# Optimization experiments

Measured on AMD Instinct MI355X. Metric: run time of the kernel, lower is better.

The kernel has to match this reference:

```python
import jax, jax.numpy as jnp
import numpy as np

B, N, C, H = 4, 2048, 1024, 16
DH = C // H
SCALE = DH ** -0.5


def setup_inputs() -> dict:
    key = jax.random.key(0)
    ks = jax.random.split(key, 5)
    s = C ** -0.5
    return {
        "x": jax.random.normal(ks[0], (B, N, C), dtype=jnp.float32),
        "Wq": jax.random.normal(ks[1], (C, C), dtype=jnp.float32) * s,
        "Wkv": jax.random.normal(ks[2], (C, 2 * C), dtype=jnp.float32) * s,
        "Wout": jax.random.normal(ks[3], (C, C), dtype=jnp.float32) * s,
        "bout": jax.random.normal(ks[4], (C,), dtype=jnp.float32) * 0.01,
    }


def reference(x, Wq, Wkv, Wout, bout):
    b, n, c = x.shape
    # projections (torch Linear: x @ W.T, here we store W already as [in,out])
    q = (x @ Wq).reshape(b, n, H, DH).transpose(0, 2, 1, 3)  # b h n d
    kv = x @ Wkv
    k, v = jnp.split(kv, 2, axis=-1)
    k = k.reshape(b, n, H, DH).transpose(0, 2, 1, 3)
    v = v.reshape(b, n, H, DH).transpose(0, 2, 1, 3)
    sim = jnp.einsum("bhnd,bhmd->bhnm", q, k) * SCALE
    attn = jax.nn.softmax(sim, axis=-1)
    out = jnp.einsum("bhnm,bhmd->bhnd", attn, v)
    out = out.transpose(0, 2, 1, 3).reshape(b, n, c)
    return out @ Wout + bout
```

## Files before the change

### kernel.cpp

```cpp
#include <hip/hip_runtime.h>
#include <stdint.h>

typedef unsigned short u16;
typedef unsigned int u32;
typedef __attribute__((ext_vector_type(8))) short bf16x8;
typedef __attribute__((ext_vector_type(8))) unsigned short u16x8;
typedef __attribute__((ext_vector_type(4))) float f32x4;

#define B_DIM 4
#define N_DIM 2048
#define C_DIM 1024
#define H_DIM 16
#define M_DIM (B_DIM * N_DIM)
#define QSCALE 0.18033688011112042f

__device__ __forceinline__ u16 f2bf(float f) {
  u32 u = __builtin_bit_cast(u32, f);
  return (u16)((u + 0x7FFFu + ((u >> 16) & 1u)) >> 16);
}

__device__ __forceinline__ void gload16(const void* g, void* l) {
  __builtin_amdgcn_global_load_lds(
      (const __attribute__((address_space(1))) u32*)g,
      (__attribute__((address_space(3))) u32*)l, 16, 0, 0);
}

__global__ void cast_bf16_kernel(const float* __restrict__ in, u16* __restrict__ out, int n4) {
  int i = blockIdx.x * blockDim.x + threadIdx.x;
  int stride = gridDim.x * blockDim.x;
  for (; i < n4; i += stride) {
    float4 v = ((const float4*)in)[i];
    ushort4 o;
    o.x = f2bf(v.x); o.y = f2bf(v.y); o.z = f2bf(v.z); o.w = f2bf(v.w);
    ((ushort4*)out)[i] = o;
  }
}

__global__ void tcast_kernel(const float* __restrict__ W, u16* __restrict__ Wt, int K, int N) {
  __shared__ float tile[32][33];
  int n0 = blockIdx.x * 32, k0 = blockIdx.y * 32;
  int tx = threadIdx.x, ty = threadIdx.y;
  #pragma unroll
  for (int i = 0; i < 32; i += 8)
    tile[ty + i][tx] = W[(size_t)(k0 + ty + i) * N + (n0 + tx)];
  __syncthreads();
  #pragma unroll
  for (int i = 0; i < 32; i += 8)
    Wt[(size_t)(n0 + ty + i) * K + (k0 + tx)] = f2bf(tile[tx][ty + i]);
}

template <int MODE>
__global__ __launch_bounds__(256) void gemm_bt_kernel(
    const u16* __restrict__ A, const u16* __restrict__ Bt, void* __restrict__ Cout,
    const float* __restrict__ bias, u16* __restrict__ vt, u16* __restrict__ aux,
    int K, int N) {
  __shared__ __align__(16) char lds[16384];
  const int tid  = threadIdx.x;
  const int lane = tid & 63, w = tid >> 6;
  const int lr = lane & 15, g = lane >> 4;
  const int m0 = blockIdx.y * 128, n0 = blockIdx.x * 128;
  const int wm = w >> 1, wn = w & 1;

  f32x4 acc[4][4] = {};
  const int nkt = K >> 5;
  const int rsub = lane >> 2;
  const int csub = lane & 3;
  for (int kt = 0; kt < nkt; ++kt) {
    #pragma unroll
    for (int j = 0; j < 2; ++j) {
      int rowblk = w * 2 + j;
      int row = rowblk * 16 + rsub;
      gload16(A  + (size_t)(m0 + row) * K + kt * 32 + csub * 8, lds + rowblk * 1024);
      gload16(Bt + (size_t)(n0 + row) * K + kt * 32 + csub * 8, lds + 8192 + rowblk * 1024);
    }
    __syncthreads();
    bf16x8 a[4], b[4];
    #pragma unroll
    for (int m = 0; m < 4; ++m)
      a[m] = *(const bf16x8*)(lds + ((wm * 64 + m * 16 + lr) * 64 + g * 16));
    #pragma unroll
    for (int n = 0; n < 4; ++n)
      b[n] = *(const bf16x8*)(lds + 8192 + ((wn * 64 + n * 16 + lr) * 64 + g * 16));
    #pragma unroll
    for (int m = 0; m < 4; ++m)
      #pragma unroll
      for (int n = 0; n < 4; ++n)
        acc[m][n] = __builtin_amdgcn_mfma_f32_16x16x32_bf16(a[m], b[n], acc[m][n], 0, 0, 0);
    __syncthreads();
  }
  #pragma unroll
  for (int m = 0; m < 4; ++m) {
    #pragma unroll
    for (int n = 0; n < 4; ++n) {
      int col  = n0 + wn * 64 + n * 16 + lr;
      int row0 = m0 + wm * 64 + m * 16 + g * 4;
      if constexpr (MODE == 1) {
        #pragma unroll
        for (int r = 0; r < 4; ++r)
          ((float*)Cout)[(size_t)(row0 + r) * N + col] = acc[m][n][r] + bias[col];
      } else {
        if (col < 1024) {
          #pragma unroll
          for (int r = 0; r < 4; ++r)
            ((u16*)Cout)[(size_t)(row0 + r) * 1024 + col] = f2bf(acc[m][n][r] * QSCALE);
        } else if (col < 2048) {
          int cc = col - 1024;
          #pragma unroll
          for (int r = 0; r < 4; ++r)
            aux[(size_t)(row0 + r) * 1024 + cc] = f2bf(acc[m][n][r]);
        } else {
          int cc = col - 2048;
          int hh = cc >> 6, d = cc & 63;
          int bb = row0 >> 11, nn = row0 & 2047;
          ushort4 pkv;
          pkv.x = f2bf(acc[m][n][0]); pkv.y = f2bf(acc[m][n][1]);
          pkv.z = f2bf(acc[m][n][2]); pkv.w = f2bf(acc[m][n][3]);
          *(ushort4*)(vt + ((size_t)(bb * 16 + hh) * 64 + d) * 2048 + nn) = pkv;
        }
      }
    }
  }
}

__global__ __launch_bounds__(256) void attn_kernel(
    const u16* __restrict__ Qb, const u16* __restrict__ Kb,
    const u16* __restrict__ Vt, u16* __restrict__ AO) {
  __shared__ __align__(16) char lds[51200];
  const int tid  = threadIdx.x;
  const int lane = tid & 63, w = tid >> 6;
  const int lr = lane & 15, g = lane >> 4;
  const int lin = blockIdx.x;
  const int nid = (lin & 7) * 128 + (lin >> 3);
  const int bh = nid >> 4;
  const int b = bh >> 4, h = bh & 15;
  const int q0 = (nid & 15) * 128 + w * 32;
  const size_t rowbase = (size_t)b * N_DIM;

  bf16x8 qf[2][2];
  #pragma unroll
  for (int qs = 0; qs < 2; ++qs)
    #pragma unroll
    for (int kb = 0; kb < 2; ++kb)
      qf[qs][kb] = *(const bf16x8*)(Qb + (rowbase + q0 + qs * 16 + lr) * C_DIM + h * 64 + kb * 32 + g * 8);

  bf16x8 onesb;
  #pragma unroll
  for (int j = 0; j < 8; ++j) onesb[j] = (short)0x3F80;

  f32x4 accO[2][4] = {};
  f32x4 accSum[2] = {};
  char* Pl = lds + 32768 + w * 4608;

  auto STAGE = [&](int kt, int buf) {
    #pragma unroll
    for (int j = 0; j < 2; ++j) {
      int c = (w * 2 + j) * 64 + lane;
      int row = c >> 3, slot = (c & 7) ^ (row & 7);
      gload16(Kb + (size_t)(rowbase + kt * 64 + row) * 1024 + h * 64 + slot * 8,
              lds + buf * 8192 + (w * 2 + j) * 1024);
      gload16(Vt + ((size_t)bh * 64 + row) * 2048 + kt * 64 + slot * 8,
              lds + 16384 + buf * 8192 + (w * 2 + j) * 1024);
    }
  };

  STAGE(0, 0);
  __syncthreads();

  for (int kt = 0; kt < N_DIM / 64; ++kt) {
    if (kt + 1 < N_DIM / 64) STAGE(kt + 1, (kt + 1) & 1);
    const char* K_ = lds + (kt & 1) * 8192;
    const char* V_ = lds + 16384 + (kt & 1) * 8192;

    bf16x8 kfr[4][2];
    #pragma unroll
    for (int kf = 0; kf < 4; ++kf)
      #pragma unroll
      for (int kb = 0; kb < 2; ++kb)
        kfr[kf][kb] = *(const bf16x8*)(K_ + (kf * 16 + lr) * 128 + (((kb * 4 + g) ^ (lr & 7)) << 4));
    f32x4 st[2][4] = {};
    #pragma unroll
    for (int qs = 0; qs < 2; ++qs)
      #pragma unroll
      for (int kf = 0; kf < 4; ++kf)
        #pragma unroll
        for (int kb = 0; kb < 2; ++kb)
          st[qs][kf] = __builtin_amdgcn_mfma_f32_16x16x32_bf16(kfr[kf][kb], qf[qs][kb], st[qs][kf], 0, 0, 0);

    #pragma unroll
    for (int qs = 0; qs < 2; ++qs) {
      #pragma unroll
      for (int kf = 0; kf < 4; ++kf) {
        float e0 = __builtin_amdgcn_exp2f(st[qs][kf][0]);
        float e1 = __builtin_amdgcn_exp2f(st[qs][kf][1]);
        float e2 = __builtin_amdgcn_exp2f(st[qs][kf][2]);
        float e3 = __builtin_amdgcn_exp2f(st[qs][kf][3]);
        u32 r0, r1;
        asm("v_cvt_pk_bf16_f32 %0, %1, %2" : "=v"(r0) : "v"(e0), "v"(e1));
        asm("v_cvt_pk_bf16_f32 %0, %1, %2" : "=v"(r1) : "v"(e2), "v"(e3));
        uint2 pk; pk.x = r0; pk.y = r1;
        *(uint2*)(Pl + (qs * 16 + lr) * 144 + kf * 32 + g * 8) = pk;
      }
    }

    bf16x8 vfr[4][2];
    #pragma unroll
    for (int nf = 0; nf < 4; ++nf)
      #pragma unroll
      for (int kb = 0; kb < 2; ++kb)
        vfr[nf][kb] = *(const bf16x8*)(V_ + (nf * 16 + lr) * 128 + (((kb * 4 + g) ^ (lr & 7)) << 4));
    #pragma unroll
    for (int qs = 0; qs < 2; ++qs) {
      #pragma unroll
      for (int kb = 0; kb < 2; ++kb) {
        bf16x8 pa = *(const bf16x8*)(Pl + (qs * 16 + lr) * 144 + kb * 64 + g * 16);
        accSum[qs] = __builtin_amdgcn_mfma_f32_16x16x32_bf16(pa, onesb, accSum[qs], 0, 0, 0);
        #pragma unroll
        for (int nf = 0; nf < 4; ++nf)
          accO[qs][nf] = __builtin_amdgcn_mfma_f32_16x16x32_bf16(pa, vfr[nf][kb], accO[qs][nf], 0, 0, 0);
      }
    }
    __syncthreads();
  }

  #pragma unroll
  for (int qs = 0; qs < 2; ++qs)
    #pragma unroll
    for (int r = 0; r < 4; ++r) {
      float inv = __builtin_amdgcn_rcpf(accSum[qs][r]);
      int q = q0 + qs * 16 + 4 * g + r;
      #pragma unroll
      for (int nf = 0; nf < 4; ++nf)
        AO[(rowbase + q) * C_DIM + h * 64 + nf * 16 + lr] = f2bf(accO[qs][nf][r] * inv);
    }
}

extern "C" void kernel_launch(void* const* d_in, const int* in_sizes, int n_in,
                              void* d_out, int out_size, void* d_ws, size_t ws_size,
                              hipStream_t stream) {
  (void)in_sizes; (void)n_in; (void)out_size; (void)ws_size;
  const float* x    = (const float*)d_in[0];
  const float* Wq   = (const float*)d_in[1];
  const float* Wkv  = (const float*)d_in[2];
  const float* Wout = (const float*)d_in[3];
  const float* bout = (const float*)d_in[4];
  float* out = (float*)d_out;

  char* ws = (char*)d_ws;
  u16* xb   = (u16*)(ws);
  u16* wqT  = (u16*)(ws + (16u << 20));
  u16* wkvT = (u16*)(ws + (18u << 20));
  u16* woT  = (u16*)(ws + (22u << 20));
  u16* q    = (u16*)(ws + (24u << 20));
  u16* kbuf = (u16*)(ws + (40u << 20));
  u16* vT   = (u16*)(ws + (56u << 20));
  u16* ao   = xb;

  cast_bf16_kernel<<<2048, 256, 0, stream>>>(x, xb, M_DIM * C_DIM / 4);
  dim3 tb(32, 8);
  tcast_kernel<<<dim3(C_DIM / 32,     C_DIM / 32), tb, 0, stream>>>(Wq,   wqT,  C_DIM, C_DIM);
  tcast_kernel<<<dim3(2 * C_DIM / 32, C_DIM / 32), tb, 0, stream>>>(Wkv,  wkvT, C_DIM, 2 * C_DIM);
  tcast_kernel<<<dim3(C_DIM / 32,     C_DIM / 32), tb, 0, stream>>>(Wout, woT,  C_DIM, C_DIM);

  gemm_bt_kernel<3><<<dim3(3 * C_DIM / 128, M_DIM / 128), 256, 0, stream>>>(
      xb, wqT, q, nullptr, vT, kbuf, C_DIM, 3 * C_DIM);

  attn_kernel<<<dim3(N_DIM / 128 * B_DIM * H_DIM), 256, 0, stream>>>(q, kbuf, vT, ao);

  gemm_bt_kernel<1><<<dim3(C_DIM / 128, M_DIM / 128), 256, 0, stream>>>(
      ao, woT, out, bout, nullptr, nullptr, C_DIM, C_DIM);
}
```

Before: 222.5 us.

## Use 32x32x16 MFMA in attention and keep P in registers instead of LDS

Switches the attention inner loop from 16x16x32 to 32x32x16 bf16 MFMA tiles. The S accumulator layout now lines up with the A-operand layout of the PV MFMA, so the exponentiated probabilities are packed straight into registers instead of going through a per-wave LDS round trip. This drops the P LDS buffer, shrinking shared memory, and V is read with split 8-byte loads to fit the new operand layout. The cost is larger accumulators per lane and more register pressure, plus different LDS access patterns for V.

```diff
diff --git a/kernel.cpp b/kernel.cpp
--- a/kernel.cpp
+++ b/kernel.cpp
@@ -4,8 +4,9 @@
 typedef unsigned short u16;
 typedef unsigned int u32;
 typedef __attribute__((ext_vector_type(8))) short bf16x8;
-typedef __attribute__((ext_vector_type(8))) unsigned short u16x8;
 typedef __attribute__((ext_vector_type(4))) float f32x4;
+typedef __attribute__((ext_vector_type(16))) float f32x16;
+typedef __attribute__((ext_vector_type(4))) u32 u32x4;
 
 #define B_DIM 4
 #define N_DIM 2048
@@ -13,6 +14,12 @@
 #define H_DIM 16
 #define M_DIM (B_DIM * N_DIM)
 #define QSCALE 0.18033688011112042f
+
+#if defined(__HIP_DEVICE_COMPILE__)
+#define MFMA32(a, b, c) __builtin_amdgcn_mfma_f32_32x32x16_bf16(a, b, c, 0, 0, 0)
+#else
+#define MFMA32(a, b, c) (c)
+#endif
 
 __device__ __forceinline__ u16 f2bf(float f) {
   u32 u = __builtin_bit_cast(u32, f);
@@ -125,10 +132,10 @@
 __global__ __launch_bounds__(256) void attn_kernel(
     const u16* __restrict__ Qb, const u16* __restrict__ Kb,
     const u16* __restrict__ Vt, u16* __restrict__ AO) {
-  __shared__ __align__(16) char lds[51200];
+  __shared__ __align__(16) char lds[32768];
   const int tid  = threadIdx.x;
   const int lane = tid & 63, w = tid >> 6;
-  const int lr = lane & 15, g = lane >> 4;
+  const int l31 = lane & 31, hi = lane >> 5;
   const int lin = blockIdx.x;
   const int nid = (lin & 7) * 128 + (lin >> 3);
   const int bh = nid >> 4;
@@ -136,20 +143,17 @@
   const int q0 = (nid & 15) * 128 + w * 32;
   const size_t rowbase = (size_t)b * N_DIM;
 
-  bf16x8 qf[2][2];
-  #pragma unroll
-  for (int qs = 0; qs < 2; ++qs)
-    #pragma unroll
-    for (int kb = 0; kb < 2; ++kb)
-      qf[qs][kb] = *(const bf16x8*)(Qb + (rowbase + q0 + qs * 16 + lr) * C_DIM + h * 64 + kb * 32 + g * 8);
-
-  bf16x8 onesb;
-  #pragma unroll
-  for (int j = 0; j < 8; ++j) onesb[j] = (short)0x3F80;
-
-  f32x4 accO[2][4] = {};
-  f32x4 accSum[2] = {};
-  char* Pl = lds + 32768 + w * 4608;
+  bf16x8 qf[4];
+  #pragma unroll
+  for (int dk = 0; dk < 4; ++dk)
+    qf[dk] = *(const bf16x8*)(Qb + (rowbase + q0 + l31) * C_DIM + h * 64 + dk * 16 + hi * 8);
+
+  bf16x8 ones8;
+  #pragma unroll
+  for (int j = 0; j < 8; ++j) ones8[j] = (short)0x3F80;
+
+  f32x16 accO[2] = {};
+  f32x16 accSum = {};
 
   auto STAGE = [&](int kt, int buf) {
     #pragma unroll
@@ -171,67 +175,56 @@
     const char* K_ = lds + (kt & 1) * 8192;
     const char* V_ = lds + 16384 + (kt & 1) * 8192;
 
-    bf16x8 kfr[4][2];
-    #pragma unroll
-    for (int kf = 0; kf < 4; ++kf)
-      #pragma unroll
-      for (int kb = 0; kb < 2; ++kb)
-        kfr[kf][kb] = *(const bf16x8*)(K_ + (kf * 16 + lr) * 128 + (((kb * 4 + g) ^ (lr & 7)) << 4));
-    f32x4 st[2][4] = {};
-    #pragma unroll
-    for (int qs = 0; qs < 2; ++qs)
-      #pragma unroll
-      for (int kf = 0; kf < 4; ++kf)
+    u32 paw[4][4];
+    #pragma unroll
+    for (int kvb = 0; kvb < 2; ++kvb) {
+      f32x16 st = {};
+      #pragma unroll
+      for (int dk = 0; dk < 4; ++dk) {
+        bf16x8 kf_ = *(const bf16x8*)(K_ + (kvb * 32 + l31) * 128 + (((2 * dk + hi) ^ (l31 & 7)) << 4));
+        st = MFMA32(kf_, qf[dk], st);
+      }
+      #pragma unroll
+      for (int t = 0; t < 2; ++t) {
+        float e[8];
         #pragma unroll
-        for (int kb = 0; kb < 2; ++kb)
-          st[qs][kf] = __builtin_amdgcn_mfma_f32_16x16x32_bf16(kfr[kf][kb], qf[qs][kb], st[qs][kf], 0, 0, 0);
-
-    #pragma unroll
-    for (int qs = 0; qs < 2; ++qs) {
-      #pragma unroll
-      for (int kf = 0; kf < 4; ++kf) {
-        float e0 = __builtin_amdgcn_exp2f(st[qs][kf][0]);
-        float e1 = __builtin_amdgcn_exp2f(st[qs][kf][1]);
-        float e2 = __builtin_amdgcn_exp2f(st[qs][kf][2]);
-        float e3 = __builtin_amdgcn_exp2f(st[qs][kf][3]);
-        u32 r0, r1;
-        asm("v_cvt_pk_bf16_f32 %0, %1, %2" : "=v"(r0) : "v"(e0), "v"(e1));
-        asm("v_cvt_pk_bf16_f32 %0, %1, %2" : "=v"(r1) : "v"(e2), "v"(e3));
-        uint2 pk; pk.x = r0; pk.y = r1;
-        *(uint2*)(Pl + (qs * 16 + lr) * 144 + kf * 32 + g * 8) = pk;
-      }
-    }
-
-    bf16x8 vfr[4][2];
-    #pragma unroll
-    for (int nf = 0; nf < 4; ++nf)
-      #pragma unroll
-      for (int kb = 0; kb < 2; ++kb)
-        vfr[nf][kb] = *(const bf16x8*)(V_ + (nf * 16 + lr) * 128 + (((kb * 4 + g) ^ (lr & 7)) << 4));
-    #pragma unroll
-    for (int qs = 0; qs < 2; ++qs) {
-      #pragma unroll
-      for (int kb = 0; kb < 2; ++kb) {
-        bf16x8 pa = *(const bf16x8*)(Pl + (qs * 16 + lr) * 144 + kb * 64 + g * 16);
-        accSum[qs] = __builtin_amdgcn_mfma_f32_16x16x32_bf16(pa, onesb, accSum[qs], 0, 0, 0);
+        for (int j = 0; j < 8; ++j) e[j] = __builtin_amdgcn_exp2f(st[t * 8 + j]);
         #pragma unroll
-        for (int nf = 0; nf < 4; ++nf)
-          accO[qs][nf] = __builtin_amdgcn_mfma_f32_16x16x32_bf16(pa, vfr[nf][kb], accO[qs][nf], 0, 0, 0);
+        for (int ww = 0; ww < 4; ++ww) {
+          u32 r_;
+          asm("v_cvt_pk_bf16_f32 %0, %1, %2" : "=v"(r_) : "v"(e[2 * ww]), "v"(e[2 * ww + 1]));
+          paw[kvb * 2 + t][ww] = r_;
+        }
+      }
+    }
+
+    #pragma unroll
+    for (int kb = 0; kb < 4; ++kb) {
+      u32x4 pk4 = {paw[kb][0], paw[kb][1], paw[kb][2], paw[kb][3]};
+      bf16x8 pab = __builtin_bit_cast(bf16x8, pk4);
+      accSum = MFMA32(pab, ones8, accSum);
+      #pragma unroll
+      for (int db = 0; db < 2; ++db) {
+        const char* vrow = V_ + (db * 32 + l31) * 128;
+        int sw = l31 & 7;
+        uint2 v0 = *(const uint2*)(vrow + (((2 * kb) ^ sw) << 4) + 8 * hi);
+        uint2 v1 = *(const uint2*)(vrow + (((2 * kb + 1) ^ sw) << 4) + 8 * hi);
+        u32x4 vv = {v0.x, v0.y, v1.x, v1.y};
+        bf16x8 vf_ = __builtin_bit_cast(bf16x8, vv);
+        accO[db] = MFMA32(pab, vf_, accO[db]);
       }
     }
     __syncthreads();
   }
 
   #pragma unroll
-  for (int qs = 0; qs < 2; ++qs)
-    #pragma unroll
-    for (int r = 0; r < 4; ++r) {
-      float inv = __builtin_amdgcn_rcpf(accSum[qs][r]);
-      int q = q0 + qs * 16 + 4 * g + r;
-      #pragma unroll
-      for (int nf = 0; nf < 4; ++nf)
-        AO[(rowbase + q) * C_DIM + h * 64 + nf * 16 + lr] = f2bf(accO[qs][nf][r] * inv);
-    }
+  for (int r = 0; r < 16; ++r) {
+    int qrow = q0 + (r & 3) + 8 * (r >> 2) + 4 * hi;
+    float inv = __builtin_amdgcn_rcpf(accSum[r]);
+    #pragma unroll
+    for (int db = 0; db < 2; ++db)
+      AO[(rowbase + qrow) * C_DIM + h * 64 + db * 32 + l31] = f2bf(accO[db][r] * inv);
+  }
 }
 
 extern "C" void kernel_launch(void* const* d_in, const int* in_sizes, int n_in,
```

Result: no change. 219.8 us (-1.2%).
